# Kernel optimization log

Measured on AMD Instinct MI355X. Metric: run time of the kernel, lower is better.

The kernel has to match this reference:

```python
import jax, jax.numpy as jnp
import numpy as np

B, LC, LQ, D = 32, 2048, 256, 256


def setup_inputs() -> dict:
    key = jax.random.key(0)
    kc, kq, kcm, kqm, kw = jax.random.split(key, 5)
    context = jax.random.normal(kc, (B, LC, D), dtype=jnp.float32)
    query = jax.random.normal(kq, (B, LQ, D), dtype=jnp.float32)
    # True = masked (matches torch masked_fill semantics)
    context_mask = jax.random.randint(kcm, (B, LC), 0, 2).astype(bool)
    query_mask = jax.random.randint(kqm, (B, LQ), 0, 2).astype(bool)
    # nn.Linear(3*dim, 1, bias=False) weight, flattened to (3D,)
    w0 = jax.random.normal(kw, (3 * D,), dtype=jnp.float32) * (1.0 / np.sqrt(3 * D))
    return {"context": context, "query": query, "context_mask": context_mask,
            "query_mask": query_mask, "w0": w0}


def reference(context, query, context_mask, query_mask, w0):
    d = context.shape[-1]
    wc, wq, wm = w0[:d], w0[d:2 * d], w0[2 * d:]
    # trilinear sim: w0 . [c, q, c*q]  ==  c.wc + q.wq + (c*wm) q^T
    sc = context @ wc                                   # (B, Lc)
    sq = query @ wq                                     # (B, Lq)
    sim = sc[:, :, None] + sq[:, None, :] + jnp.einsum(
        'bcd,bqd->bcq', context * wm, query)            # (B, Lc, Lq)
    mask = context_mask[:, :, None] | query_mask[:, None, :]
    sim = jnp.where(mask, jnp.float32(-1e30), sim)
    S = jax.nn.softmax(sim, axis=-1)                    # row softmax over Lq
    SS = jax.nn.softmax(sim, axis=1)                    # col softmax over Lc
    S = jnp.nan_to_num(S)
    SS = jnp.nan_to_num(SS)
    A = jnp.einsum('bcq,bqd->bcd', S, query)            # (B, Lc, D)
    T = jnp.einsum('bkq,bkd->bqd', SS, context)         # SS^T @ context, (B, Lq, D)
    Bmat = jnp.einsum('bcq,bqd->bcd', S, T)             # (B, Lc, D)
    return (A, Bmat)
```

## Files before the change

kernel.cpp:

```cpp
#include <hip/hip_runtime.h>

#define B_  32
#define LC_ 2048
#define LQ_ 256
#define D_  256
#define NEGH (-30000.0f)
#define MASKF (-100000.0f)

typedef _Float16 f16;
typedef _Float16 f16x4 __attribute__((ext_vector_type(4)));
typedef _Float16 f16x8 __attribute__((ext_vector_type(8)));
typedef float    f32x4 __attribute__((ext_vector_type(4)));

__global__ __launch_bounds__(256) void k_prep(
    const float* __restrict__ ctx, const float* __restrict__ qry,
    const float* __restrict__ w0,
    const int* __restrict__ cmask, const int* __restrict__ qmask,
    f16* __restrict__ ctx16, f16* __restrict__ qrywm16,
    float* __restrict__ scm, float* __restrict__ sqm)
{
    const int lane = threadIdx.x & 63;
    const int wave = threadIdx.x >> 6;
    const int row  = blockIdx.x * 4 + wave;
    const int NC = B_ * LC_;
    if (row < NC) {
        float4 v = *(const float4*)(ctx + (long long)row * D_ + lane * 4);
        f16x4 h; h[0] = (f16)v.x; h[1] = (f16)v.y; h[2] = (f16)v.z; h[3] = (f16)v.w;
        *(f16x4*)(ctx16 + (long long)row * D_ + lane * 4) = h;
        float4 wc = *(const float4*)(w0 + lane * 4);
        float s = v.x*wc.x + v.y*wc.y + v.z*wc.z + v.w*wc.w;
        #pragma unroll
        for (int off = 32; off > 0; off >>= 1) s += __shfl_down(s, off, 64);
        if (lane == 0) scm[row] = cmask[row] ? MASKF : s;
    } else {
        int r = row - NC;
        float4 v = *(const float4*)(qry + (long long)r * D_ + lane * 4);
        float4 wm = *(const float4*)(w0 + 2 * D_ + lane * 4);
        f16x4 h;
        h[0] = (f16)(v.x * wm.x); h[1] = (f16)(v.y * wm.y);
        h[2] = (f16)(v.z * wm.z); h[3] = (f16)(v.w * wm.w);
        *(f16x4*)(qrywm16 + (long long)r * D_ + lane * 4) = h;
        float4 wq = *(const float4*)(w0 + D_ + lane * 4);
        float s = v.x*wq.x + v.y*wq.y + v.z*wq.z + v.w*wq.w;
        #pragma unroll
        for (int off = 32; off > 0; off >>= 1) s += __shfl_down(s, off, 64);
        if (lane == 0) sqm[r] = qmask[r] ? MASKF : s;
    }
}

__global__ __launch_bounds__(256) void k_tq(
    const float* __restrict__ in, f16* __restrict__ out)
{
    __shared__ float tile[64 * 65];
    const int b = blockIdx.z;
    const int r0 = blockIdx.x * 64, c0 = blockIdx.y * 64;
    const int t = threadIdx.x;
    const float* ib = in + (long long)b * LQ_ * D_;
    #pragma unroll
    for (int p = 0; p < 4; ++p) {
        int r = (t >> 4) + p * 16;
        int cb = (t & 15) * 4;
        float4 v = *(const float4*)(ib + (long long)(r0 + r) * D_ + c0 + cb);
        tile[r * 65 + cb + 0] = v.x;
        tile[r * 65 + cb + 1] = v.y;
        tile[r * 65 + cb + 2] = v.z;
        tile[r * 65 + cb + 3] = v.w;
    }
    __syncthreads();
    f16* ob = out + (long long)b * 512 * LQ_;
    #pragma unroll
    for (int p = 0; p < 4; ++p) {
        int c = (t >> 4) + p * 16;
        int rb = (t & 15) * 4;
        f16x4 h;
        h[0] = (f16)tile[(rb + 0) * 65 + c];
        h[1] = (f16)tile[(rb + 1) * 65 + c];
        h[2] = (f16)tile[(rb + 2) * 65 + c];
        h[3] = (f16)tile[(rb + 3) * 65 + c];
        *(f16x4*)(ob + (long long)(c0 + c) * LQ_ + r0 + rb) = h;
    }
}

#define LDA1 40
__global__ __launch_bounds__(512, 4) void k_g1(
    const f16* __restrict__ ctx16, const f16* __restrict__ qrywm16,
    const float* __restrict__ scm, const float* __restrict__ sqm,
    f16* __restrict__ sim16, f16* __restrict__ p16,
    float* __restrict__ rowinvl,
    float* __restrict__ pm, float* __restrict__ pl)
{
    __shared__ f16 As[128 * LDA1];
    __shared__ f16 Bs[256 * LDA1];
    __shared__ float rowpm[4][128], rowps[4][128];
    __shared__ float colpm[2][256], colps[2][256];
    __shared__ float rowmax_s[128], colmax_s[256];
    const int b = blockIdx.z;
    const int c0 = blockIdx.x * 128;
    const int t = threadIdx.x, lane = t & 63, wv = t >> 6;
    const int wm_off = (wv >> 2) * 64, wn_off = (wv & 3) * 64;
    const f16* Ab = ctx16 + ((long long)b * LC_ + c0) * D_;
    const f16* Bb = qrywm16 + (long long)b * LQ_ * D_;
    const int srow = t >> 2, scg = (t & 3) * 8;
    f32x4 acc[4][4] = {};
    f16x8 ha, hb0, hb1;
    ha  = *(const f16x8*)(Ab + (long long)srow * D_ + scg);
    hb0 = *(const f16x8*)(Bb + (long long)srow * D_ + scg);
    hb1 = *(const f16x8*)(Bb + (long long)(srow + 128) * D_ + scg);
    for (int k0 = 0; k0 < D_; k0 += 32) {
        *(f16x8*)(As + srow * LDA1 + scg) = ha;
        *(f16x8*)(Bs + srow * LDA1 + scg) = hb0;
        *(f16x8*)(Bs + (srow + 128) * LDA1 + scg) = hb1;
        if (k0 + 32 < D_) {
            ha  = *(const f16x8*)(Ab + (long long)srow * D_ + k0 + 32 + scg);
            hb0 = *(const f16x8*)(Bb + (long long)srow * D_ + k0 + 32 + scg);
            hb1 = *(const f16x8*)(Bb + (long long)(srow + 128) * D_ + k0 + 32 + scg);
        }
        __syncthreads();
        f16x8 af[4], bf[4];
        #pragma unroll
        for (int i = 0; i < 4; ++i)
            af[i] = *(const f16x8*)(As + (wm_off + i * 16 + (lane & 15)) * LDA1 + (lane >> 4) * 8);
        #pragma unroll
        for (int j = 0; j < 4; ++j)
            bf[j] = *(const f16x8*)(Bs + (wn_off + j * 16 + (lane & 15)) * LDA1 + (lane >> 4) * 8);
        #pragma unroll
        for (int i = 0; i < 4; ++i)
            #pragma unroll
            for (int j = 0; j < 4; ++j)
                acc[i][j] = __builtin_amdgcn_mfma_f32_16x16x32_f16(af[i], bf[j], acc[i][j], 0, 0, 0);
        __syncthreads();
    }
    float sqv[4];
    #pragma unroll
    for (int j = 0; j < 4; ++j)
        sqv[j] = sqm[b * LQ_ + wn_off + j * 16 + (lane & 15)];
    float scv[4][4];
    #pragma unroll
    for (int i = 0; i < 4; ++i)
        #pragma unroll
        for (int r = 0; r < 4; ++r)
            scv[i][r] = scm[b * LC_ + c0 + wm_off + i * 16 + (lane >> 4) * 4 + r];
    float rmax[4][4], cmax[4];
    #pragma unroll
    for (int i = 0; i < 4; ++i)
        #pragma unroll
        for (int r = 0; r < 4; ++r) rmax[i][r] = -INFINITY;
    #pragma unroll
    for (int j = 0; j < 4; ++j) cmax[j] = -INFINITY;
    #pragma unroll
    for (int i = 0; i < 4; ++i) {
        #pragma unroll
        for (int r = 0; r < 4; ++r) {
            int c = c0 + wm_off + i * 16 + (lane >> 4) * 4 + r;
            f16* orow = sim16 + ((long long)b * LC_ + c) * LQ_ + wn_off + (lane & 15);
            #pragma unroll
            for (int j = 0; j < 4; ++j) {
                float val = fmaxf(acc[i][j][r] + scv[i][r] + sqv[j], NEGH);
                f16 hh = (f16)val;
                orow[j * 16] = hh;
                float vr = (float)hh;
                rmax[i][r] = fmaxf(rmax[i][r], vr);
                cmax[j]    = fmaxf(cmax[j], vr);
            }
        }
    }
    #pragma unroll
    for (int i = 0; i < 4; ++i)
        #pragma unroll
        for (int r = 0; r < 4; ++r) {
            rmax[i][r] = fmaxf(rmax[i][r], __shfl_xor(rmax[i][r], 1, 64));
            rmax[i][r] = fmaxf(rmax[i][r], __shfl_xor(rmax[i][r], 2, 64));
            rmax[i][r] = fmaxf(rmax[i][r], __shfl_xor(rmax[i][r], 4, 64));
            rmax[i][r] = fmaxf(rmax[i][r], __shfl_xor(rmax[i][r], 8, 64));
        }
    #pragma unroll
    for (int j = 0; j < 4; ++j) {
        cmax[j] = fmaxf(cmax[j], __shfl_xor(cmax[j], 16, 64));
        cmax[j] = fmaxf(cmax[j], __shfl_xor(cmax[j], 32, 64));
    }
    if ((lane & 15) == 0) {
        #pragma unroll
        for (int i = 0; i < 4; ++i)
            #pragma unroll
            for (int r = 0; r < 4; ++r)
                rowpm[wv & 3][wm_off + i * 16 + (lane >> 4) * 4 + r] = rmax[i][r];
    }
    if (lane < 16) {
        #pragma unroll
        for (int j = 0; j < 4; ++j) colpm[wv >> 2][wn_off + j * 16 + lane] = cmax[j];
    }
    __syncthreads();
    if (t < 128)
        rowmax_s[t] = fmaxf(fmaxf(rowpm[0][t], rowpm[1][t]), fmaxf(rowpm[2][t], rowpm[3][t]));
    if (t < 256)
        colmax_s[t] = fmaxf(colpm[0][t], colpm[1][t]);
    __syncthreads();
    float rmf[4][4], cmf[4];
    #pragma unroll
    for (int i = 0; i < 4; ++i)
        #pragma unroll
        for (int r = 0; r < 4; ++r)
            rmf[i][r] = rowmax_s[wm_off + i * 16 + (lane >> 4) * 4 + r];
    #pragma unroll
    for (int j = 0; j < 4; ++j) cmf[j] = colmax_s[wn_off + j * 16 + (lane & 15)];
    float rsum[4][4] = {}, csum[4] = {};
    #pragma unroll
    for (int i = 0; i < 4; ++i) {
        #pragma unroll
        for (int r = 0; r < 4; ++r) {
            int c = c0 + wm_off + i * 16 + (lane >> 4) * 4 + r;
            f16* prow = p16 + ((long long)b * LC_ + c) * LQ_ + wn_off + (lane & 15);
            #pragma unroll
            for (int j = 0; j < 4; ++j) {
                float val = fmaxf(acc[i][j][r] + scv[i][r] + sqv[j], NEGH);
                float vr = (float)(f16)val;
                float er = __expf(vr - rmf[i][r]);
                prow[j * 16] = (f16)er;
                rsum[i][r] += er;
                csum[j]    += __expf(vr - cmf[j]);
            }
        }
    }
    #pragma unroll
    for (int i = 0; i < 4; ++i)
        #pragma unroll
        for (int r = 0; r < 4; ++r) {
            rsum[i][r] += __shfl_xor(rsum[i][r], 1, 64);
            rsum[i][r] += __shfl_xor(rsum[i][r], 2, 64);
            rsum[i][r] += __shfl_xor(rsum[i][r], 4, 64);
            rsum[i][r] += __shfl_xor(rsum[i][r], 8, 64);
        }
    #pragma unroll
    for (int j = 0; j < 4; ++j) {
        csum[j] += __shfl_xor(csum[j], 16, 64);
        csum[j] += __shfl_xor(csum[j], 32, 64);
    }
    if ((lane & 15) == 0) {
        #pragma unroll
        for (int i = 0; i < 4; ++i)
            #pragma unroll
            for (int r = 0; r < 4; ++r)
                rowps[wv & 3][wm_off + i * 16 + (lane >> 4) * 4 + r] = rsum[i][r];
    }
    if (lane < 16) {
        #pragma unroll
        for (int j = 0; j < 4; ++j) colps[wv >> 2][wn_off + j * 16 + lane] = csum[j];
    }
    __syncthreads();
    if (t < 128) {
        float l = rowps[0][t] + rowps[1][t] + rowps[2][t] + rowps[3][t];
        rowinvl[b * LC_ + c0 + t] = 1.0f / l;
    }
    if (t < 256) {
        int idx = (b * 16 + blockIdx.x) * LQ_ + t;
        pm[idx] = colmax_s[t];
        pl[idx] = colps[0][t] + colps[1][t];
    }
}

__global__ __launch_bounds__(256) void k_colreduce(
    const float* __restrict__ pm, const float* __restrict__ pl,
    float* __restrict__ colm, float* __restrict__ colinvl)
{
    const int col = blockIdx.x * 256 + threadIdx.x;
    const int b = col >> 8, q = col & 255;
    float M = -INFINITY, L = 0.f;
    for (int ch = 0; ch < 16; ++ch) {
        int idx = (b * 16 + ch) * LQ_ + q;
        float m = pm[idx], l = pl[idx];
        float nM = fmaxf(M, m);
        L = L * __expf(M - nM) + l * __expf(m - nM);
        M = nM;
    }
    colm[col] = M; colinvl[col] = 1.0f / L;
}

#define LDA3 66
#define G3SPLIT 4
#define G3CHUNK (LC_ / G3SPLIT)
__global__ __launch_bounds__(256) void k_g3(
    const f16* __restrict__ ctx16, const f16* __restrict__ sim16,
    const float* __restrict__ colm, float* __restrict__ Tpart)
{
    __shared__ f16 As[128 * LDA3];
    __shared__ f16 Bs[64 * LDA3];
    __shared__ float colm_s[64];
    const int b = blockIdx.x;
    const int combo = blockIdx.y;
    const int qt = combo & 3, dh = combo >> 2;
    const int q0 = qt * 64, d0 = dh * 128;
    const int cbeg = blockIdx.z * G3CHUNK;
    const int t = threadIdx.x, lane = t & 63, wv = t >> 6;
    const int wm_off = (wv >> 1) * 64, wn_off = (wv & 1) * 32;
    if (t < 64) colm_s[t] = colm[b * LQ_ + q0 + t];
    __syncthreads();
    const f16* Ab = ctx16 + (long long)b * LC_ * D_;
    const f16* Sb = sim16 + (long long)b * LC_ * LQ_;
    f32x4 acc[4][2] = {};
    const int acc_ = t >> 4, ad8 = (t & 15) * 8;
    const int bcc = t >> 3, bq8 = (t & 7) * 8;
    f16x8 ha[4], hb[2];
    #pragma unroll
    for (int p = 0; p < 4; ++p)
        ha[p] = *(const f16x8*)(Ab + (long long)(cbeg + acc_ + p * 16) * D_ + d0 + ad8);
    #pragma unroll
    for (int p = 0; p < 2; ++p)
        hb[p] = *(const f16x8*)(Sb + (long long)(cbeg + bcc + p * 32) * LQ_ + q0 + bq8);
    for (int c0 = cbeg; c0 < cbeg + G3CHUNK; c0 += 64) {
        #pragma unroll
        for (int p = 0; p < 4; ++p) {
            int cc = acc_ + p * 16;
            #pragma unroll
            for (int j = 0; j < 8; ++j)
                As[(ad8 + j) * LDA3 + cc] = ha[p][j];
        }
        #pragma unroll
        for (int p = 0; p < 2; ++p) {
            int cc = bcc + p * 32;
            #pragma unroll
            for (int j = 0; j < 8; ++j)
                Bs[(bq8 + j) * LDA3 + cc] = (f16)__expf((float)hb[p][j] - colm_s[bq8 + j]);
        }
        if (c0 + 64 < cbeg + G3CHUNK) {
            #pragma unroll
            for (int p = 0; p < 4; ++p)
                ha[p] = *(const f16x8*)(Ab + (long long)(c0 + 64 + acc_ + p * 16) * D_ + d0 + ad8);
            #pragma unroll
            for (int p = 0; p < 2; ++p)
                hb[p] = *(const f16x8*)(Sb + (long long)(c0 + 64 + bcc + p * 32) * LQ_ + q0 + bq8);
        }
        __syncthreads();
        #pragma unroll
        for (int kk = 0; kk < 64; kk += 32) {
            f16x8 af[4], bf[2];
            #pragma unroll
            for (int i = 0; i < 4; ++i)
                af[i] = *(const f16x8*)(As + (wm_off + i * 16 + (lane & 15)) * LDA3 + kk + (lane >> 4) * 8);
            #pragma unroll
            for (int j = 0; j < 2; ++j)
                bf[j] = *(const f16x8*)(Bs + (wn_off + j * 16 + (lane & 15)) * LDA3 + kk + (lane >> 4) * 8);
            #pragma unroll
            for (int i = 0; i < 4; ++i)
                #pragma unroll
                for (int j = 0; j < 2; ++j)
                    acc[i][j] = __builtin_amdgcn_mfma_f32_16x16x32_f16(af[i], bf[j], acc[i][j], 0, 0, 0);
        }
        __syncthreads();
    }
    float* Tb = Tpart + ((long long)blockIdx.z * B_ + b) * (LQ_ * D_);
    #pragma unroll
    for (int i = 0; i < 4; ++i) {
        #pragma unroll
        for (int r = 0; r < 4; ++r) {
            int d = d0 + wm_off + i * 16 + (lane >> 4) * 4 + r;
            float* orow = Tb + (long long)d * LQ_ + q0 + wn_off + (lane & 15);
            #pragma unroll
            for (int j = 0; j < 2; ++j)
                orow[j * 16] = acc[i][j][r];
        }
    }
}

__global__ __launch_bounds__(256) void k_bnorm(
    const float* __restrict__ Tpart, const float* __restrict__ colinvl,
    f16* __restrict__ Bcat)
{
    const long long i4 = ((long long)blockIdx.x * 256 + threadIdx.x) * 4;
    const int q = (int)(i4 & 255);
    const int d = (int)((i4 >> 8) & 255);
    const int b = (int)(i4 >> 16);
    float4 s = *(const float4*)(Tpart + i4);
    #pragma unroll
    for (int p = 1; p < G3SPLIT; ++p) {
        float4 v = *(const float4*)(Tpart + (long long)p * (B_ * LQ_ * D_) + i4);
        s.x += v.x; s.y += v.y; s.z += v.z; s.w += v.w;
    }
    float4 ci = *(const float4*)(colinvl + b * LQ_ + q);
    f16x4 h;
    h[0] = (f16)(s.x * ci.x); h[1] = (f16)(s.y * ci.y);
    h[2] = (f16)(s.z * ci.z); h[3] = (f16)(s.w * ci.w);
    *(f16x4*)(Bcat + (long long)b * 512 * LQ_ + (long long)(256 + d) * LQ_ + q) = h;
}

__global__ __launch_bounds__(256, 4) void k_g23(
    const f16* __restrict__ p16, const float* __restrict__ rowinvl,
    const f16* __restrict__ Bcat,
    float* __restrict__ outA, float* __restrict__ outB)
{
    __shared__ f16 As[128 * LDA1];
    __shared__ f16 Bs[128 * LDA1];
    const int b = blockIdx.z;
    const int c0 = blockIdx.x * 128, n0 = blockIdx.y * 128;
    const int t = threadIdx.x, lane = t & 63, wv = t >> 6;
    const int wm_off = (wv >> 1) * 64, wn_off = (wv & 1) * 64;
    const f16* Ab = p16 + ((long long)b * LC_ + c0) * LQ_;
    const f16* Bb = Bcat + ((long long)b * 512 + n0) * LQ_;
    const int srow = t >> 2, scg = (t & 3) * 8;
    f32x4 acc[4][4] = {};
    f16x8 ha[2], hb[2];
    #pragma unroll
    for (int p = 0; p < 2; ++p) {
        int r = srow + p * 64;
        ha[p] = *(const f16x8*)(Ab + (long long)r * LQ_ + scg);
        hb[p] = *(const f16x8*)(Bb + (long long)r * LQ_ + scg);
    }
    for (int k0 = 0; k0 < LQ_; k0 += 32) {
        #pragma unroll
        for (int p = 0; p < 2; ++p) {
            int r = srow + p * 64;
            *(f16x8*)(As + r * LDA1 + scg) = ha[p];
            *(f16x8*)(Bs + r * LDA1 + scg) = hb[p];
        }
        if (k0 + 32 < LQ_) {
            #pragma unroll
            for (int p = 0; p < 2; ++p) {
                int r = srow + p * 64;
                ha[p] = *(const f16x8*)(Ab + (long long)r * LQ_ + k0 + 32 + scg);
                hb[p] = *(const f16x8*)(Bb + (long long)r * LQ_ + k0 + 32 + scg);
            }
        }
        __syncthreads();
        f16x8 af[4], bf[4];
        #pragma unroll
        for (int i = 0; i < 4; ++i)
            af[i] = *(const f16x8*)(As + (wm_off + i * 16 + (lane & 15)) * LDA1 + (lane >> 4) * 8);
        #pragma unroll
        for (int j = 0; j < 4; ++j)
            bf[j] = *(const f16x8*)(Bs + (wn_off + j * 16 + (lane & 15)) * LDA1 + (lane >> 4) * 8);
        #pragma unroll
        for (int i = 0; i < 4; ++i)
            #pragma unroll
            for (int j = 0; j < 4; ++j)
                acc[i][j] = __builtin_amdgcn_mfma_f32_16x16x32_f16(af[i], bf[j], acc[i][j], 0, 0, 0);
        __syncthreads();
    }
    float* outp = (n0 < 256) ? outA : outB;
    const int nbase = (n0 < 256) ? n0 : (n0 - 256);
    #pragma unroll
    for (int i = 0; i < 4; ++i) {
        #pragma unroll
        for (int r = 0; r < 4; ++r) {
            int c = c0 + wm_off + i * 16 + (lane >> 4) * 4 + r;
            float ri = rowinvl[b * LC_ + c];
            float* orow = outp + ((long long)b * LC_ + c) * D_ + nbase + wn_off + (lane & 15);
            #pragma unroll
            for (int j = 0; j < 4; ++j)
                orow[j * 16] = acc[i][j][r] * ri;
        }
    }
}

extern "C" void kernel_launch(void* const* d_in, const int* in_sizes, int n_in,
                              void* d_out, int out_size, void* d_ws, size_t ws_size,
                              hipStream_t stream) {
    const float* ctx   = (const float*)d_in[0];
    const float* qry   = (const float*)d_in[1];
    const int*   cmask = (const int*)d_in[2];
    const int*   qmask = (const int*)d_in[3];
    const float* w0    = (const float*)d_in[4];
    float* out = (float*)d_out;

    char* w = (char*)d_ws;
    float* scm     = (float*)w;  w += (long long)65536 * 4;
    float* sqm     = (float*)w;  w += (long long)8192 * 4;
    float* rowinvl = (float*)w;  w += (long long)65536 * 4;
    float* colm    = (float*)w;  w += (long long)8192 * 4;
    float* colinvl = (float*)w;  w += (long long)8192 * 4;
    float* pm      = (float*)w;  w += (long long)524288 * 4;
    float* pl      = (float*)w;  w += (long long)524288 * 4;
    f16*   sim16   = (f16*)w;    w += (long long)16777216 * 2;
    f16*   p16     = (f16*)w;    w += (long long)16777216 * 2;
    f16*   ctx16   = (f16*)w;    w += (long long)16777216 * 2;
    f16*   qrywm16 = (f16*)w;    w += (long long)2097152 * 2;
    f16*   Bcat    = (f16*)w;    w += (long long)4194304 * 2;
    float* Tpart   = (float*)w;  w += (long long)G3SPLIT * 2097152 * 4;

    k_prep<<<18432, 256, 0, stream>>>(ctx, qry, w0, cmask, qmask, ctx16, qrywm16, scm, sqm);
    k_tq<<<dim3(4, 4, 32), 256, 0, stream>>>(qry, Bcat);
    k_g1<<<dim3(16, 1, 32), 512, 0, stream>>>(ctx16, qrywm16, scm, sqm,
        sim16, p16, rowinvl, pm, pl);
    k_colreduce<<<32, 256, 0, stream>>>(pm, pl, colm, colinvl);
    k_g3<<<dim3(32, 8, G3SPLIT), 256, 0, stream>>>(ctx16, sim16, colm, Tpart);
    k_bnorm<<<2048, 256, 0, stream>>>(Tpart, colinvl, Bcat);
    k_g23<<<dim3(16, 4, 32), 256, 0, stream>>>(p16, rowinvl, Bcat,
        out, out + (long long)B_ * LC_ * D_);
}
```

Before: 312.7 us.

## Fuse context conversion into first GEMM and feed column GEMM transposed probabilities

Result: no change. 312.6 us (-0.0%).

```diff
diff --git a/kernel.cpp b/kernel.cpp
--- a/kernel.cpp
+++ b/kernel.cpp
@@ -12,40 +12,25 @@
 typedef _Float16 f16x8 __attribute__((ext_vector_type(8)));
 typedef float    f32x4 __attribute__((ext_vector_type(4)));
 
-__global__ __launch_bounds__(256) void k_prep(
-    const float* __restrict__ ctx, const float* __restrict__ qry,
-    const float* __restrict__ w0,
-    const int* __restrict__ cmask, const int* __restrict__ qmask,
-    f16* __restrict__ ctx16, f16* __restrict__ qrywm16,
-    float* __restrict__ scm, float* __restrict__ sqm)
+__global__ __launch_bounds__(256) void k_prepq(
+    const float* __restrict__ qry, const float* __restrict__ w0,
+    const int* __restrict__ qmask,
+    f16* __restrict__ qrywm16, float* __restrict__ sqm)
 {
     const int lane = threadIdx.x & 63;
     const int wave = threadIdx.x >> 6;
-    const int row  = blockIdx.x * 4 + wave;
-    const int NC = B_ * LC_;
-    if (row < NC) {
-        float4 v = *(const float4*)(ctx + (long long)row * D_ + lane * 4);
-        f16x4 h; h[0] = (f16)v.x; h[1] = (f16)v.y; h[2] = (f16)v.z; h[3] = (f16)v.w;
-        *(f16x4*)(ctx16 + (long long)row * D_ + lane * 4) = h;
-        float4 wc = *(const float4*)(w0 + lane * 4);
-        float s = v.x*wc.x + v.y*wc.y + v.z*wc.z + v.w*wc.w;
-        #pragma unroll
-        for (int off = 32; off > 0; off >>= 1) s += __shfl_down(s, off, 64);
-        if (lane == 0) scm[row] = cmask[row] ? MASKF : s;
-    } else {
-        int r = row - NC;
-        float4 v = *(const float4*)(qry + (long long)r * D_ + lane * 4);
-        float4 wm = *(const float4*)(w0 + 2 * D_ + lane * 4);
-        f16x4 h;
-        h[0] = (f16)(v.x * wm.x); h[1] = (f16)(v.y * wm.y);
-        h[2] = (f16)(v.z * wm.z); h[3] = (f16)(v.w * wm.w);
-        *(f16x4*)(qrywm16 + (long long)r * D_ + lane * 4) = h;
-        float4 wq = *(const float4*)(w0 + D_ + lane * 4);
-        float s = v.x*wq.x + v.y*wq.y + v.z*wq.z + v.w*wq.w;
-        #pragma unroll
-        for (int off = 32; off > 0; off >>= 1) s += __shfl_down(s, off, 64);
-        if (lane == 0) sqm[r] = qmask[r] ? MASKF : s;
-    }
+    const int r = blockIdx.x * 4 + wave;
+    float4 v = *(const float4*)(qry + (long long)r * D_ + lane * 4);
+    float4 wm = *(const float4*)(w0 + 2 * D_ + lane * 4);
+    f16x4 h;
+    h[0] = (f16)(v.x * wm.x); h[1] = (f16)(v.y * wm.y);
+    h[2] = (f16)(v.z * wm.z); h[3] = (f16)(v.w * wm.w);
+    *(f16x4*)(qrywm16 + (long long)r * D_ + lane * 4) = h;
+    float4 wq = *(const float4*)(w0 + D_ + lane * 4);
+    float s = v.x*wq.x + v.y*wq.y + v.z*wq.z + v.w*wq.w;
+    #pragma unroll
+    for (int off = 32; off > 0; off >>= 1) s += __shfl_down(s, off, 64);
+    if (lane == 0) sqm[r] = qmask[r] ? MASKF : s;
 }
 
 __global__ __launch_bounds__(256) void k_tq(
@@ -83,14 +68,17 @@
 
 #define LDA1 40
 __global__ __launch_bounds__(512, 4) void k_g1(
-    const f16* __restrict__ ctx16, const f16* __restrict__ qrywm16,
-    const float* __restrict__ scm, const float* __restrict__ sqm,
-    f16* __restrict__ sim16, f16* __restrict__ p16,
-    float* __restrict__ rowinvl,
+    const float* __restrict__ ctx, const f16* __restrict__ qrywm16,
+    const float* __restrict__ w0, const int* __restrict__ cmask,
+    const float* __restrict__ sqm,
+    f16* __restrict__ ctxT16, f16* __restrict__ p16, f16* __restrict__ pT16,
+    float* __restrict__ rowm, float* __restrict__ rowinvl,
     float* __restrict__ pm, float* __restrict__ pl)
 {
     __shared__ f16 As[128 * LDA1];
     __shared__ f16 Bs[256 * LDA1];
+    __shared__ float wc_s[256];
+    __shared__ float scm_s[128];
     __shared__ float rowpm[4][128], rowps[4][128];
     __shared__ float colpm[2][256], colps[2][256];
     __shared__ float rowmax_s[128], colmax_s[256];
@@ -98,23 +86,27 @@
     const int c0 = blockIdx.x * 128;
     const int t = threadIdx.x, lane = t & 63, wv = t >> 6;
     const int wm_off = (wv >> 2) * 64, wn_off = (wv & 3) * 64;
-    const f16* Ab = ctx16 + ((long long)b * LC_ + c0) * D_;
+    const float* Ab = ctx + ((long long)b * LC_ + c0) * D_;
     const f16* Bb = qrywm16 + (long long)b * LQ_ * D_;
     const int srow = t >> 2, scg = (t & 3) * 8;
+    const int td = t & 31, tcc = t >> 5;
+    if (t < 256) wc_s[t] = w0[t];
+    __syncthreads();
     f32x4 acc[4][4] = {};
-    f16x8 ha, hb0, hb1;
-    ha  = *(const f16x8*)(Ab + (long long)srow * D_ + scg);
-    hb0 = *(const f16x8*)(Bb + (long long)srow * D_ + scg);
-    hb1 = *(const f16x8*)(Bb + (long long)(srow + 128) * D_ + scg);
+    float scdot = 0.f;
     for (int k0 = 0; k0 < D_; k0 += 32) {
+        float4 a0 = *(const float4*)(Ab + (long long)srow * D_ + k0 + scg);
+        float4 a1 = *(const float4*)(Ab + (long long)srow * D_ + k0 + scg + 4);
+        f16x8 ha;
+        ha[0] = (f16)a0.x; ha[1] = (f16)a0.y; ha[2] = (f16)a0.z; ha[3] = (f16)a0.w;
+        ha[4] = (f16)a1.x; ha[5] = (f16)a1.y; ha[6] = (f16)a1.z; ha[7] = (f16)a1.w;
+        scdot += a0.x * wc_s[k0 + scg + 0] + a0.y * wc_s[k0 + scg + 1]
+               + a0.z * wc_s[k0 + scg + 2] + a0.w * wc_s[k0 + scg + 3]
+               + a1.x * wc_s[k0 + scg + 4] + a1.y * wc_s[k0 + scg + 5]
+               + a1.z * wc_s[k0 + scg + 6] + a1.w * wc_s[k0 + scg + 7];
         *(f16x8*)(As + srow * LDA1 + scg) = ha;
-        *(f16x8*)(Bs + srow * LDA1 + scg) = hb0;
-        *(f16x8*)(Bs + (srow + 128) * LDA1 + scg) = hb1;
-        if (k0 + 32 < D_) {
-            ha  = *(const f16x8*)(Ab + (long long)srow * D_ + k0 + 32 + scg);
-            hb0 = *(const f16x8*)(Bb + (long long)srow * D_ + k0 + 32 + scg);
-            hb1 = *(const f16x8*)(Bb + (long long)(srow + 128) * D_ + k0 + 32 + scg);
-        }
+        *(f16x8*)(Bs + srow * LDA1 + scg) = *(const f16x8*)(Bb + (long long)srow * D_ + k0 + scg);
+        *(f16x8*)(Bs + (srow + 128) * LDA1 + scg) = *(const f16x8*)(Bb + (long long)(srow + 128) * D_ + k0 + scg);
         __syncthreads();
         f16x8 af[4], bf[4];
         #pragma unroll
@@ -128,8 +120,20 @@
             #pragma unroll
             for (int j = 0; j < 4; ++j)
                 acc[i][j] = __builtin_amdgcn_mfma_f32_16x16x32_f16(af[i], bf[j], acc[i][j], 0, 0, 0);
-        __syncthreads();
-    }
+        {
+            f16x8 hT;
+            #pragma unroll
+            for (int j = 0; j < 8; ++j)
+                hT[j] = As[(tcc * 8 + j) * LDA1 + td];
+            *(f16x8*)(ctxT16 + ((long long)b * D_ + k0 + td) * LC_ + c0 + tcc * 8) = hT;
+        }
+        __syncthreads();
+    }
+    scdot += __shfl_xor(scdot, 1, 64);
+    scdot += __shfl_xor(scdot, 2, 64);
+    if ((t & 3) == 0)
+        scm_s[srow] = cmask[b * LC_ + c0 + srow] ? MASKF : scdot;
+    __syncthreads();
     float sqv[4];
     #pragma unroll
     for (int j = 0; j < 4; ++j)
@@ -139,7 +143,7 @@
     for (int i = 0; i < 4; ++i)
         #pragma unroll
         for (int r = 0; r < 4; ++r)
-            scv[i][r] = scm[b * LC_ + c0 + wm_off + i * 16 + (lane >> 4) * 4 + r];
+            scv[i][r] = scm_s[wm_off + i * 16 + (lane >> 4) * 4 + r];
     float rmax[4][4], cmax[4];
     #pragma unroll
     for (int i = 0; i < 4; ++i)
@@ -151,14 +155,10 @@
     for (int i = 0; i < 4; ++i) {
         #pragma unroll
         for (int r = 0; r < 4; ++r) {
-            int c = c0 + wm_off + i * 16 + (lane >> 4) * 4 + r;
-            f16* orow = sim16 + ((long long)b * LC_ + c) * LQ_ + wn_off + (lane & 15);
             #pragma unroll
             for (int j = 0; j < 4; ++j) {
                 float val = fmaxf(acc[i][j][r] + scv[i][r] + sqv[j], NEGH);
-                f16 hh = (f16)val;
-                orow[j * 16] = hh;
-                float vr = (float)hh;
+                float vr = (float)(f16)val;
                 rmax[i][r] = fmaxf(rmax[i][r], vr);
                 cmax[j]    = fmaxf(cmax[j], vr);
             }
@@ -212,10 +212,13 @@
             f16* prow = p16 + ((long long)b * LC_ + c) * LQ_ + wn_off + (lane & 15);
             #pragma unroll
             for (int j = 0; j < 4; ++j) {
+                int q = wn_off + j * 16 + (lane & 15);
                 float val = fmaxf(acc[i][j][r] + scv[i][r] + sqv[j], NEGH);
                 float vr = (float)(f16)val;
                 float er = __expf(vr - rmf[i][r]);
-                prow[j * 16] = (f16)er;
+                f16 hp = (f16)er;
+                prow[j * 16] = hp;
+                pT16[((long long)b * LQ_ + q) * LC_ + c] = hp;
                 rsum[i][r] += er;
                 csum[j]    += __expf(vr - cmf[j]);
             }
@@ -249,6 +252,7 @@
     __syncthreads();
     if (t < 128) {
         float l = rowps[0][t] + rowps[1][t] + rowps[2][t] + rowps[3][t];
+        rowm[b * LC_ + c0 + t]    = rowmax_s[t];
         rowinvl[b * LC_ + c0 + t] = 1.0f / l;
     }
     if (t < 256) {
@@ -275,15 +279,17 @@
     colm[col] = M; colinvl[col] = 1.0f / L;
 }
 
-#define LDA3 66
+#define LDA3 72
 #define G3SPLIT 4
 #define G3CHUNK (LC_ / G3SPLIT)
 __global__ __launch_bounds__(256) void k_g3(
-    const f16* __restrict__ ctx16, const f16* __restrict__ sim16,
-    const float* __restrict__ colm, float* __restrict__ Tpart)
+    const f16* __restrict__ ctxT16, const f16* __restrict__ pT16,
+    const float* __restrict__ rowm, const float* __restrict__ colm,
+    float* __restrict__ Tpart)
 {
     __shared__ f16 As[128 * LDA3];
     __shared__ f16 Bs[64 * LDA3];
+    __shared__ float rowm_s[G3CHUNK];
     __shared__ float colm_s[64];
     const int b = blockIdx.x;
     const int combo = blockIdx.y;
@@ -292,42 +298,45 @@
     const int cbeg = blockIdx.z * G3CHUNK;
     const int t = threadIdx.x, lane = t & 63, wv = t >> 6;
     const int wm_off = (wv >> 1) * 64, wn_off = (wv & 1) * 32;
+    for (int i = t; i < G3CHUNK; i += 256) rowm_s[i] = rowm[b * LC_ + cbeg + i];
     if (t < 64) colm_s[t] = colm[b * LQ_ + q0 + t];
     __syncthreads();
-    const f16* Ab = ctx16 + (long long)b * LC_ * D_;
-    const f16* Sb = sim16 + (long long)b * LC_ * LQ_;
+    const f16* Ab = ctxT16 + ((long long)b * D_ + d0) * LC_;
+    const f16* Pb = pT16 + ((long long)b * LQ_ + q0) * LC_;
+    const int ar = t >> 3, acg = (t & 7) * 8;
     f32x4 acc[4][2] = {};
-    const int acc_ = t >> 4, ad8 = (t & 15) * 8;
-    const int bcc = t >> 3, bq8 = (t & 7) * 8;
     f16x8 ha[4], hb[2];
     #pragma unroll
     for (int p = 0; p < 4; ++p)
-        ha[p] = *(const f16x8*)(Ab + (long long)(cbeg + acc_ + p * 16) * D_ + d0 + ad8);
+        ha[p] = *(const f16x8*)(Ab + (long long)(ar + p * 32) * LC_ + cbeg + acg);
     #pragma unroll
     for (int p = 0; p < 2; ++p)
-        hb[p] = *(const f16x8*)(Sb + (long long)(cbeg + bcc + p * 32) * LQ_ + q0 + bq8);
+        hb[p] = *(const f16x8*)(Pb + (long long)(ar + p * 32) * LC_ + cbeg + acg);
     for (int c0 = cbeg; c0 < cbeg + G3CHUNK; c0 += 64) {
         #pragma unroll
-        for (int p = 0; p < 4; ++p) {
-            int cc = acc_ + p * 16;
-            #pragma unroll
-            for (int j = 0; j < 8; ++j)
-                As[(ad8 + j) * LDA3 + cc] = ha[p][j];
-        }
+        for (int p = 0; p < 4; ++p)
+            *(f16x8*)(As + (ar + p * 32) * LDA3 + acg) = ha[p];
         #pragma unroll
         for (int p = 0; p < 2; ++p) {
-            int cc = bcc + p * 32;
-            #pragma unroll
-            for (int j = 0; j < 8; ++j)
-                Bs[(bq8 + j) * LDA3 + cc] = (f16)__expf((float)hb[p][j] - colm_s[bq8 + j]);
+            float cmq = colm_s[ar + p * 32];
+            f16x8 e;
+            if (cmq < -29000.f) {
+                #pragma unroll
+                for (int j = 0; j < 8; ++j) e[j] = (f16)1.0f;
+            } else {
+                #pragma unroll
+                for (int j = 0; j < 8; ++j)
+                    e[j] = (f16)((float)hb[p][j] * __expf(rowm_s[(c0 - cbeg) + acg + j] - cmq));
+            }
+            *(f16x8*)(Bs + (ar + p * 32) * LDA3 + acg) = e;
         }
         if (c0 + 64 < cbeg + G3CHUNK) {
             #pragma unroll
             for (int p = 0; p < 4; ++p)
-                ha[p] = *(const f16x8*)(Ab + (long long)(c0 + 64 + acc_ + p * 16) * D_ + d0 + ad8);
+                ha[p] = *(const f16x8*)(Ab + (long long)(ar + p * 32) * LC_ + c0 + 64 + acg);
             #pragma unroll
             for (int p = 0; p < 2; ++p)
-                hb[p] = *(const f16x8*)(Sb + (long long)(c0 + 64 + bcc + p * 32) * LQ_ + q0 + bq8);
+                hb[p] = *(const f16x8*)(Pb + (long long)(ar + p * 32) * LC_ + c0 + 64 + acg);
         }
         __syncthreads();
         #pragma unroll
@@ -461,26 +470,26 @@
     float* out = (float*)d_out;
 
     char* w = (char*)d_ws;
-    float* scm     = (float*)w;  w += (long long)65536 * 4;
     float* sqm     = (float*)w;  w += (long long)8192 * 4;
+    float* rowm    = (float*)w;  w += (long long)65536 * 4;
     float* rowinvl = (float*)w;  w += (long long)65536 * 4;
     float* colm    = (float*)w;  w += (long long)8192 * 4;
     float* colinvl = (float*)w;  w += (long long)8192 * 4;
     float* pm      = (float*)w;  w += (long long)524288 * 4;
     float* pl      = (float*)w;  w += (long long)524288 * 4;
-    f16*   sim16   = (f16*)w;    w += (long long)16777216 * 2;
     f16*   p16     = (f16*)w;    w += (long long)16777216 * 2;
-    f16*   ctx16   = (f16*)w;    w += (long long)16777216 * 2;
+    f16*   pT16    = (f16*)w;    w += (long long)16777216 * 2;
+    f16*   ctxT16  = (f16*)w;    w += (long long)16777216 * 2;
     f16*   qrywm16 = (f16*)w;    w += (long long)2097152 * 2;
     f16*   Bcat    = (f16*)w;    w += (long long)4194304 * 2;
     float* Tpart   = (float*)w;  w += (long long)G3SPLIT * 2097152 * 4;
 
-    k_prep<<<18432, 256, 0, stream>>>(ctx, qry, w0, cmask, qmask, ctx16, qrywm16, scm, sqm);
+    k_prepq<<<2048, 256, 0, stream>>>(qry, w0, qmask, qrywm16, sqm);
     k_tq<<<dim3(4, 4, 32), 256, 0, stream>>>(qry, Bcat);
-    k_g1<<<dim3(16, 1, 32), 512, 0, stream>>>(ctx16, qrywm16, scm, sqm,
-        sim16, p16, rowinvl, pm, pl);
+    k_g1<<<dim3(16, 1, 32), 512, 0, stream>>>(ctx, qrywm16, w0, cmask, sqm,
+        ctxT16, p16, pT16, rowm, rowinvl, pm, pl);
     k_colreduce<<<32, 256, 0, stream>>>(pm, pl, colm, colinvl);
-    k_g3<<<dim3(32, 8, G3SPLIT), 256, 0, stream>>>(ctx16, sim16, colm, Tpart);
+    k_g3<<<dim3(32, 8, G3SPLIT), 256, 0, stream>>>(ctxT16, pT16, rowm, colm, Tpart);
     k_bnorm<<<2048, 256, 0, stream>>>(Tpart, colinvl, Bcat);
     k_g23<<<dim3(16, 4, 32), 256, 0, stream>>>(p16, rowinvl, Bcat,
         out, out + (long long)B_ * LC_ * D_);
```
